# Optimization experiments

Measured on AMD Instinct MI355X. Metric: run time of the kernel, lower is better.

## Reference

```python
import jax, jax.numpy as jnp
import numpy as np

N, C_IN, H, W = 32, 128, 56, 56
C_OUT, KH, KW = 256, 3, 3
STRIDE = (1, 1)
PAD = (1, 1)


def setup_inputs() -> dict:
    key = jax.random.key(0)
    k_x, k_w, k_b = jax.random.split(key, 3)
    x = jax.random.normal(k_x, (N, C_IN, H, W), dtype=jnp.float32)
    # kaiming_uniform-like scale for weight, uniform bias in [-1/sqrt(fan_in), 1/sqrt(fan_in)]
    fan_in = C_IN * KH * KW
    bound_w = float(np.sqrt(6.0 / ((1 + 5.0) * fan_in)))  # kaiming_uniform a=sqrt(5)
    weight = jax.random.uniform(k_w, (C_OUT, C_IN, KH, KW), dtype=jnp.float32,
                                minval=-bound_w, maxval=bound_w)
    bound_b = float(1.0 / np.sqrt(fan_in))
    bias = jax.random.uniform(k_b, (C_OUT,), dtype=jnp.float32,
                              minval=-bound_b, maxval=bound_b)
    return {"x": x, "weight": weight, "bias": bias}


def reference(x, weight, bias):
    # Faithful math of the im2col conv: zero padding (ph,pw)=(1,1), stride 1,
    # groups=1 -> identical to a standard cross-correlation conv2d + bias.
    out = jax.lax.conv_general_dilated(
        x, weight,
        window_strides=STRIDE,
        padding=[(PAD[0], PAD[0]), (PAD[1], PAD[1])],
        dimension_numbers=("NCHW", "OIHW", "NCHW"),
    )
    return out + bias[None, :, None, None]
```

## Files before the change

kernel.cpp:

```cpp
#include <hip/hip_runtime.h>


#define NB   32
#define CIN  128
#define HH   56
#define WWD  56
#define COUT 256
#define HWP  3136
#define KTOT 1152
#define MTOT 100352

typedef __bf16 bf16x8 __attribute__((ext_vector_type(8)));
typedef float  f32x4  __attribute__((ext_vector_type(4)));
typedef unsigned short u16;
typedef u16 u16x4 __attribute__((ext_vector_type(4)));
typedef u16 u16x8 __attribute__((ext_vector_type(8)));

__device__ __forceinline__ u16 f2b(float f) {
  unsigned u = __float_as_uint(f);
  u += 0x7fffu + ((u >> 16) & 1u);
  return (u16)(u >> 16);
}

__device__ __forceinline__ void load_lds16(const void* g, void* l) {
  __builtin_amdgcn_global_load_lds(
      (const __attribute__((address_space(1))) unsigned int*)g,
      (__attribute__((address_space(3))) unsigned int*)l, 16, 0, 0);
}

__global__ __launch_bounds__(256) void k_transpose_x(const float* __restrict__ x,
                                                     u16* __restrict__ xt) {
  __shared__ u16 tile[64][68];
  const int n  = blockIdx.z;
  const int p0 = blockIdx.x * 64;
  const int c0 = blockIdx.y * 64;
  const int t  = threadIdx.x;

  const float* xp = x + (size_t)n * CIN * HWP + (size_t)c0 * HWP + p0;
  const int pl = (t & 15) * 4;
  const int cr = t >> 4;
#pragma unroll
  for (int j = 0; j < 4; ++j) {
    int c = cr + j * 16;
    f32x4 v = *(const f32x4*)&xp[(size_t)c * HWP + pl];
    u16x4 h;
    h[0] = f2b(v[0]); h[1] = f2b(v[1]); h[2] = f2b(v[2]); h[3] = f2b(v[3]);
    *(u16x4*)&tile[c][pl] = h;
  }
  __syncthreads();
  u16* xo = xt + (size_t)n * HWP * CIN + (size_t)p0 * CIN + c0;
  const int ch = (t & 7) * 8;
  const int pr = t >> 3;
#pragma unroll
  for (int j = 0; j < 2; ++j) {
    int p = pr + j * 32;
    u16x8 o;
#pragma unroll
    for (int i = 0; i < 8; ++i) o[i] = tile[ch + i][p];
    *(u16x8*)&xo[(size_t)p * CIN + ch] = o;
  }
}

__global__ __launch_bounds__(256) void k_transform_w(const float* __restrict__ w,
                                                     u16* __restrict__ Wt,
                                                     u16* __restrict__ zb) {
  int o = blockIdx.x * 256 + threadIdx.x;
  if (o < COUT * KTOT) {
    int co  = o / KTOT;
    int rem = o - co * KTOT;
    int kk  = rem >> 7;
    int ci  = rem & 127;
    int kh  = kk / 3;
    int kw  = kk - kh * 3;
    Wt[o] = f2b(w[(((size_t)co * CIN + ci) * 3 + kh) * 3 + kw]);
  }
  if (blockIdx.x == 0 && threadIdx.x < 128) zb[threadIdx.x] = 0;
}

__global__ __launch_bounds__(256, 4) void k_conv_gemm(
    const u16* __restrict__ xt, const u16* __restrict__ Wt,
    const u16* __restrict__ zb, const float* __restrict__ bias,
    float* __restrict__ out) {
  __shared__ u16 lW[128 * 64];
  __shared__ u16 lX[128 * 64];

  const int tid  = threadIdx.x;
  const int wave = tid >> 6;
  const int lane = tid & 63;
  const int m0   = blockIdx.x * 128;
  const int co0  = blockIdx.y * 128;

  const int wrow = (wave >> 1) * 64;
  const int wcol = (wave & 1) * 64;

  const int rsub = lane >> 3;
  const int pso  = (((lane & 7) ^ rsub)) * 8;

  int soh[4], sow[4], sbase[4];
#pragma unroll
  for (int c = 0; c < 4; ++c) {
    int chunk = wave * 4 + c;
    int m = m0 + chunk * 8 + rsub;
    int n = m / HWP;
    int s = m - n * HWP;
    int oh = s / WWD;
    int ow = s - oh * WWD;
    soh[c] = oh; sow[c] = ow;
    sbase[c] = n * HWP + oh * WWD + ow;
  }

  f32x4 acc[4][4];
#pragma unroll
  for (int i = 0; i < 4; ++i)
#pragma unroll
    for (int j = 0; j < 4; ++j) acc[i][j] = (f32x4){0.f, 0.f, 0.f, 0.f};

  const int r  = lane & 15;
  const int q  = lane >> 4;
  const int r7 = r & 7;

  for (int kt = 0; kt < 18; ++kt) {
    const int ksp = kt >> 1;
    const int kh  = ksp / 3;
    const int kw  = ksp - kh * 3;
    const int ci0 = (kt & 1) << 6;
    const int kg  = kt << 6;

    __syncthreads();
#pragma unroll
    for (int c = 0; c < 4; ++c) {
      int rowW = wave * 32 + c * 8;
      const u16* g = Wt + (size_t)(co0 + rowW + rsub) * KTOT + kg + pso;
      load_lds16(g, &lW[rowW * 64]);
    }
#pragma unroll
    for (int c = 0; c < 4; ++c) {
      int ih = soh[c] + kh - 1;
      int iw = sow[c] + kw - 1;
      bool valid = ((unsigned)ih < HH) && ((unsigned)iw < WWD);
      const u16* g = valid
          ? xt + (size_t)(sbase[c] + (kh - 1) * WWD + (kw - 1)) * CIN + ci0 + pso
          : zb + pso;
      load_lds16(g, &lX[(wave * 32 + c * 8) * 64]);
    }
    __syncthreads();

#pragma unroll
    for (int kk = 0; kk < 2; ++kk) {
      bf16x8 a[4], b[4];
      const int sw = ((kk * 4 + q) ^ r7) * 8;
#pragma unroll
      for (int ti = 0; ti < 4; ++ti)
        a[ti] = *(const bf16x8*)(&lW[(wrow + ti * 16 + r) * 64 + sw]);
#pragma unroll
      for (int tj = 0; tj < 4; ++tj)
        b[tj] = *(const bf16x8*)(&lX[(wcol + tj * 16 + r) * 64 + sw]);
#pragma unroll
      for (int ti = 0; ti < 4; ++ti)
#pragma unroll
        for (int tj = 0; tj < 4; ++tj)
          acc[ti][tj] =
              __builtin_amdgcn_mfma_f32_16x16x32_bf16(a[ti], b[tj], acc[ti][tj], 0, 0, 0);
    }
  }

#pragma unroll
  for (int tj = 0; tj < 4; ++tj) {
    int m = m0 + wcol + tj * 16 + r;
    int n = m / HWP;
    int s = m - n * HWP;
#pragma unroll
    for (int ti = 0; ti < 4; ++ti) {
      f32x4 v = acc[ti][tj];
#pragma unroll
      for (int e = 0; e < 4; ++e) {
        int co = co0 + wrow + ti * 16 + q * 4 + e;
        out[((size_t)n * COUT + co) * HWP + s] = v[e] + bias[co];
      }
    }
  }
}

extern "C" void kernel_launch(void* const* d_in, const int* in_sizes, int n_in,
                              void* d_out, int out_size, void* d_ws, size_t ws_size,
                              hipStream_t stream) {
  const float* x    = (const float*)d_in[0];
  const float* w    = (const float*)d_in[1];
  const float* bias = (const float*)d_in[2];
  float* out        = (float*)d_out;

  u16* xt = (u16*)d_ws;
  u16* Wt = xt + (size_t)NB * HWP * CIN;
  u16* zb = Wt + (size_t)COUT * KTOT;

  k_transform_w<<<dim3(1152), dim3(256), 0, stream>>>(w, Wt, zb);
  k_transpose_x<<<dim3(49, 2, 32), dim3(256), 0, stream>>>(x, xt);
  k_conv_gemm<<<dim3(784, 2), dim3(256), 0, stream>>>(xt, Wt, zb, bias, out);
}
```

Measured before the change: 207.6 us.

## Load weights straight from global into registers and use two-wave blocks

New measurement: 241.5 us. 1.16x slower.

```diff
diff --git a/kernel.cpp b/kernel.cpp
--- a/kernel.cpp
+++ b/kernel.cpp
@@ -77,11 +77,10 @@
   if (blockIdx.x == 0 && threadIdx.x < 128) zb[threadIdx.x] = 0;
 }
 
-__global__ __launch_bounds__(256, 4) void k_conv_gemm(
+__global__ __launch_bounds__(128, 2) void k_conv_gemm(
     const u16* __restrict__ xt, const u16* __restrict__ Wt,
     const u16* __restrict__ zb, const float* __restrict__ bias,
     float* __restrict__ out) {
-  __shared__ u16 lW[128 * 64];
   __shared__ u16 lX[128 * 64];
 
   const int tid  = threadIdx.x;
@@ -89,84 +88,80 @@
   const int lane = tid & 63;
   const int m0   = blockIdx.x * 128;
   const int co0  = blockIdx.y * 128;
-
-  const int wrow = (wave >> 1) * 64;
-  const int wcol = (wave & 1) * 64;
+  const int wco  = co0 + wave * 64;
 
   const int rsub = lane >> 3;
-  const int pso  = (((lane & 7) ^ rsub)) * 8;
+  const int pso  = ((lane & 7) ^ rsub) * 8;
+  const int mbase = m0 + wave * 64 + rsub;
 
-  int soh[4], sow[4], sbase[4];
+  unsigned flags = 0;
 #pragma unroll
-  for (int c = 0; c < 4; ++c) {
-    int chunk = wave * 4 + c;
-    int m = m0 + chunk * 8 + rsub;
-    int n = m / HWP;
-    int s = m - n * HWP;
+  for (int c = 0; c < 8; ++c) {
+    int m  = mbase + 8 * c;
+    int s  = m % HWP;
     int oh = s / WWD;
     int ow = s - oh * WWD;
-    soh[c] = oh; sow[c] = ow;
-    sbase[c] = n * HWP + oh * WWD + ow;
+    unsigned f = (unsigned)(oh == 0) | ((unsigned)(oh == HH - 1) << 1) |
+                 ((unsigned)(ow == 0) << 2) | ((unsigned)(ow == WWD - 1) << 3);
+    flags |= f << (4 * c);
   }
 
-  f32x4 acc[4][4];
+  f32x4 acc[4][8];
 #pragma unroll
   for (int i = 0; i < 4; ++i)
 #pragma unroll
-    for (int j = 0; j < 4; ++j) acc[i][j] = (f32x4){0.f, 0.f, 0.f, 0.f};
+    for (int j = 0; j < 8; ++j) acc[i][j] = (f32x4){0.f, 0.f, 0.f, 0.f};
 
   const int r  = lane & 15;
   const int q  = lane >> 4;
   const int r7 = r & 7;
+  const u16* wrow0 = Wt + (size_t)(wco + r) * KTOT + q * 8;
 
   for (int kt = 0; kt < 18; ++kt) {
     const int ksp = kt >> 1;
     const int kh  = ksp / 3;
     const int kw  = ksp - kh * 3;
     const int ci0 = (kt & 1) << 6;
-    const int kg  = kt << 6;
+    const int doff  = (kh - 1) * WWD + (kw - 1);
+    const unsigned imask = (unsigned)(kh == 0) | ((unsigned)(kh == 2) << 1) |
+                           ((unsigned)(kw == 0) << 2) | ((unsigned)(kw == 2) << 3);
 
     __syncthreads();
 #pragma unroll
-    for (int c = 0; c < 4; ++c) {
-      int rowW = wave * 32 + c * 8;
-      const u16* g = Wt + (size_t)(co0 + rowW + rsub) * KTOT + kg + pso;
-      load_lds16(g, &lW[rowW * 64]);
-    }
-#pragma unroll
-    for (int c = 0; c < 4; ++c) {
-      int ih = soh[c] + kh - 1;
-      int iw = sow[c] + kw - 1;
-      bool valid = ((unsigned)ih < HH) && ((unsigned)iw < WWD);
-      const u16* g = valid
-          ? xt + (size_t)(sbase[c] + (kh - 1) * WWD + (kw - 1)) * CIN + ci0 + pso
-          : zb + pso;
-      load_lds16(g, &lX[(wave * 32 + c * 8) * 64]);
+    for (int c = 0; c < 8; ++c) {
+      int chunk = wave * 8 + c;
+      bool invalid = ((flags >> (4 * c)) & imask) != 0;
+      const u16* g = invalid
+          ? zb + pso
+          : xt + (size_t)(mbase + 8 * c + doff) * CIN + ci0 + pso;
+      load_lds16(g, &lX[chunk * 8 * 64]);
     }
     __syncthreads();
 
 #pragma unroll
     for (int kk = 0; kk < 2; ++kk) {
-      bf16x8 a[4], b[4];
+      const u16* wp = wrow0 + kt * 64 + kk * 32;
+      bf16x8 a[4];
+#pragma unroll
+      for (int ti = 0; ti < 4; ++ti)
+        a[ti] = *(const bf16x8*)(wp + (size_t)ti * 16 * KTOT);
+      bf16x8 b[8];
       const int sw = ((kk * 4 + q) ^ r7) * 8;
 #pragma unroll
-      for (int ti = 0; ti < 4; ++ti)
-        a[ti] = *(const bf16x8*)(&lW[(wrow + ti * 16 + r) * 64 + sw]);
-#pragma unroll
-      for (int tj = 0; tj < 4; ++tj)
-        b[tj] = *(const bf16x8*)(&lX[(wcol + tj * 16 + r) * 64 + sw]);
+      for (int tj = 0; tj < 8; ++tj)
+        b[tj] = *(const bf16x8*)(&lX[(tj * 16 + r) * 64 + sw]);
 #pragma unroll
       for (int ti = 0; ti < 4; ++ti)
 #pragma unroll
-        for (int tj = 0; tj < 4; ++tj)
+        for (int tj = 0; tj < 8; ++tj)
           acc[ti][tj] =
               __builtin_amdgcn_mfma_f32_16x16x32_bf16(a[ti], b[tj], acc[ti][tj], 0, 0, 0);
     }
   }
 
 #pragma unroll
-  for (int tj = 0; tj < 4; ++tj) {
-    int m = m0 + wcol + tj * 16 + r;
+  for (int tj = 0; tj < 8; ++tj) {
+    int m = m0 + tj * 16 + r;
     int n = m / HWP;
     int s = m - n * HWP;
 #pragma unroll
@@ -174,7 +169,7 @@
       f32x4 v = acc[ti][tj];
 #pragma unroll
       for (int e = 0; e < 4; ++e) {
-        int co = co0 + wrow + ti * 16 + q * 4 + e;
+        int co = wco + ti * 16 + q * 4 + e;
         out[((size_t)n * COUT + co) * HWP + s] = v[e] + bias[co];
       }
     }
@@ -195,5 +190,5 @@
 
   k_transform_w<<<dim3(1152), dim3(256), 0, stream>>>(w, Wt, zb);
   k_transpose_x<<<dim3(49, 2, 32), dim3(256), 0, stream>>>(x, xt);
-  k_conv_gemm<<<dim3(784, 2), dim3(256), 0, stream>>>(xt, Wt, zb, bias, out);
+  k_conv_gemm<<<dim3(784, 2), dim3(128), 0, stream>>>(xt, Wt, zb, bias, out);
 }
```

## Remap conv GEMM blocks, precompute gather pointers, pair LDS reads in transpose

Applied to the files above, without the earlier changes.

Measured after the change: 211.4 us. No clear change (+1.8%).

```diff
diff --git a/kernel.cpp b/kernel.cpp
--- a/kernel.cpp
+++ b/kernel.cpp
@@ -30,7 +30,7 @@
 
 __global__ __launch_bounds__(256) void k_transpose_x(const float* __restrict__ x,
                                                      u16* __restrict__ xt) {
-  __shared__ u16 tile[64][68];
+  __shared__ u16 tile[64 * 68];
   const int n  = blockIdx.z;
   const int p0 = blockIdx.x * 64;
   const int c0 = blockIdx.y * 64;
@@ -45,20 +45,21 @@
     f32x4 v = *(const f32x4*)&xp[(size_t)c * HWP + pl];
     u16x4 h;
     h[0] = f2b(v[0]); h[1] = f2b(v[1]); h[2] = f2b(v[2]); h[3] = f2b(v[3]);
-    *(u16x4*)&tile[c][pl] = h;
+    *(u16x4*)&tile[c * 68 + pl] = h;
   }
   __syncthreads();
   u16* xo = xt + (size_t)n * HWP * CIN + (size_t)p0 * CIN + c0;
   const int ch = (t & 7) * 8;
-  const int pr = t >> 3;
-#pragma unroll
-  for (int j = 0; j < 2; ++j) {
-    int p = pr + j * 32;
-    u16x8 o;
-#pragma unroll
-    for (int i = 0; i < 8; ++i) o[i] = tile[ch + i][p];
-    *(u16x8*)&xo[(size_t)p * CIN + ch] = o;
-  }
+  const int p2 = (t >> 3) * 2;
+  u16x8 o0, o1;
+#pragma unroll
+  for (int i = 0; i < 8; ++i) {
+    unsigned pair = *(const unsigned*)&tile[(ch + i) * 68 + p2];
+    o0[i] = (u16)(pair & 0xffffu);
+    o1[i] = (u16)(pair >> 16);
+  }
+  *(u16x8*)&xo[(size_t)p2 * CIN + ch] = o0;
+  *(u16x8*)&xo[(size_t)(p2 + 1) * CIN + ch] = o1;
 }
 
 __global__ __launch_bounds__(256) void k_transform_w(const float* __restrict__ w,
@@ -87,27 +88,32 @@
   const int tid  = threadIdx.x;
   const int wave = tid >> 6;
   const int lane = tid & 63;
-  const int m0   = blockIdx.x * 128;
-  const int co0  = blockIdx.y * 128;
+  const int id  = blockIdx.x;
+  const int m0  = (((id >> 4) << 3) | (id & 7)) * 128;
+  const int co0 = ((id >> 3) & 1) * 128;
 
   const int wrow = (wave >> 1) * 64;
   const int wcol = (wave & 1) * 64;
 
   const int rsub = lane >> 3;
-  const int pso  = (((lane & 7) ^ rsub)) * 8;
-
-  int soh[4], sow[4], sbase[4];
+  const int pso  = ((lane & 7) ^ rsub) * 8;
+
+  const u16* bx[4];
+  const u16* bw[4];
+  unsigned flags = 0;
 #pragma unroll
   for (int c = 0; c < 4; ++c) {
-    int chunk = wave * 4 + c;
-    int m = m0 + chunk * 8 + rsub;
-    int n = m / HWP;
-    int s = m - n * HWP;
+    int m  = m0 + (wave * 4 + c) * 8 + rsub;
+    int s  = m % HWP;
     int oh = s / WWD;
     int ow = s - oh * WWD;
-    soh[c] = oh; sow[c] = ow;
-    sbase[c] = n * HWP + oh * WWD + ow;
-  }
+    unsigned f = (unsigned)(oh == 0) | ((unsigned)(oh == HH - 1) << 1) |
+                 ((unsigned)(ow == 0) << 2) | ((unsigned)(ow == WWD - 1) << 3);
+    flags |= f << (4 * c);
+    bx[c] = xt + (size_t)m * CIN + pso;
+    bw[c] = Wt + (size_t)(co0 + wave * 32 + c * 8 + rsub) * KTOT + pso;
+  }
+  const u16* zp = zb + pso;
 
   f32x4 acc[4][4];
 #pragma unroll
@@ -123,24 +129,20 @@
     const int ksp = kt >> 1;
     const int kh  = ksp / 3;
     const int kw  = ksp - kh * 3;
-    const int ci0 = (kt & 1) << 6;
-    const int kg  = kt << 6;
+    const int koff = ((kh - 1) * WWD + (kw - 1)) * CIN + ((kt & 1) << 6);
+    const unsigned imask = (unsigned)(kh == 0) | ((unsigned)(kh == 2) << 1) |
+                           ((unsigned)(kw == 0) << 2) | ((unsigned)(kw == 2) << 3);
 
     __syncthreads();
 #pragma unroll
     for (int c = 0; c < 4; ++c) {
       int rowW = wave * 32 + c * 8;
-      const u16* g = Wt + (size_t)(co0 + rowW + rsub) * KTOT + kg + pso;
-      load_lds16(g, &lW[rowW * 64]);
+      load_lds16(bw[c] + kt * 64, &lW[rowW * 64]);
     }
 #pragma unroll
     for (int c = 0; c < 4; ++c) {
-      int ih = soh[c] + kh - 1;
-      int iw = sow[c] + kw - 1;
-      bool valid = ((unsigned)ih < HH) && ((unsigned)iw < WWD);
-      const u16* g = valid
-          ? xt + (size_t)(sbase[c] + (kh - 1) * WWD + (kw - 1)) * CIN + ci0 + pso
-          : zb + pso;
+      bool invalid = ((flags >> (4 * c)) & imask) != 0;
+      const u16* g = invalid ? zp : (bx[c] + koff);
       load_lds16(g, &lX[(wave * 32 + c * 8) * 64]);
     }
     __syncthreads();
@@ -195,5 +197,5 @@
 
   k_transform_w<<<dim3(1152), dim3(256), 0, stream>>>(w, Wt, zb);
   k_transpose_x<<<dim3(49, 2, 32), dim3(256), 0, stream>>>(x, xt);
-  k_conv_gemm<<<dim3(784, 2), dim3(256), 0, stream>>>(xt, Wt, zb, bias, out);
-}
+  k_conv_gemm<<<dim3(1568), dim3(256), 0, stream>>>(xt, Wt, zb, bias, out);
+}
```
